# Kernel optimization log

Measured on AMD Instinct MI355X. Metric: run time of the kernel, lower is better.

## Reference

```python
import jax, jax.numpy as jnp
import numpy as np
from jax import lax

EPS = 1e-5

def _layernorm(x, g, b):
    m = x.mean(-1, keepdims=True)
    v = ((x - m) ** 2).mean(-1, keepdims=True)
    return (x - m) * lax.rsqrt(v + EPS) * g + b

def _batchnorm(x, g, b):
    # x: [N, C, L]; training-mode batch statistics (torch BatchNorm1d default)
    m = x.mean((0, 2), keepdims=True)
    v = ((x - m) ** 2).mean((0, 2), keepdims=True)
    return (x - m) * lax.rsqrt(v + EPS) * g[None, :, None] + b[None, :, None]

def _conv1d(x, w, bias, stride):
    y = lax.conv_general_dilated(x, w, window_strides=(stride,), padding='VALID',
                                 dimension_numbers=('NCH', 'OIH', 'NCH'))
    return y + bias[None, :, None]

def setup_inputs() -> dict:
    key = jax.random.key(0)
    ks = jax.random.split(key, 22)
    B, C, L = 512, 12, 5000
    NF, HID, LAT = 32, 64, 32
    def w(k, shape, fan_in):
        return jax.random.normal(k, shape, jnp.float32) * (1.0 / np.sqrt(fan_in))
    return {
        'x': jax.random.normal(ks[0], (B, C, L), jnp.float32),
        'c1w': w(ks[1], (32, C, 50), C * 50), 'c1b': jnp.zeros((32,), jnp.float32),
        'bn1g': jnp.ones((32,), jnp.float32), 'bn1b': jnp.zeros((32,), jnp.float32),
        'c2w': w(ks[2], (NF, 32, 25), 32 * 25), 'c2b': jnp.zeros((NF,), jnp.float32),
        'bn2g': jnp.ones((NF,), jnp.float32), 'bn2b': jnp.zeros((NF,), jnp.float32),
        'Wi': w(ks[3], (LAT, NF), NF) * 0.5, 'bi': jnp.zeros((LAT,), jnp.float32),
        'ln1g': jnp.ones((LAT,), jnp.float32), 'ln1b': jnp.zeros((LAT,), jnp.float32),
        'Wh': w(ks[4], (HID, LAT), LAT) * 0.5, 'bh': jnp.zeros((HID,), jnp.float32),
        'ln2g': jnp.ones((HID,), jnp.float32), 'ln2b': jnp.zeros((HID,), jnp.float32),
        'Wr': w(ks[5], (LAT, HID), HID) * 0.5, 'br': jnp.zeros((LAT,), jnp.float32),
        'Wo': w(ks[6], (LAT, LAT), LAT), 'bo': jnp.zeros((LAT,), jnp.float32),
    }

def reference(x, c1w, c1b, bn1g, bn1b, c2w, c2b, bn2g, bn2b,
              Wi, bi, ln1g, ln1b, Wh, bh, ln2g, ln2b, Wr, br, Wo, bo):
    # CNN front-end: [B,12,5000] -> [B,32,496] -> [B,32,95]
    h = jax.nn.relu(_batchnorm(_conv1d(x, c1w, c1b, 10), bn1g, bn1b))
    h = jax.nn.relu(_batchnorm(_conv1d(h, c2w, c2b, 5), bn2g, bn2b))
    feats = h.transpose(2, 0, 1)  # [T, B, NF]
    # input_proj + ln1 have no dependence on the recurrent state -> hoist out of loop
    xt_all = _layernorm(jnp.einsum('tbf,lf->tbl', feats, Wi) + bi, ln1g, ln1b)  # [T,B,LAT]

    def step(hstate, xt):
        combined = xt + hstate
        hp = jax.nn.relu(combined @ Wh.T + bh)      # [B, HID]
        hp = _layernorm(hp, ln2g, ln2b)
        hnew = jnp.tanh(hp @ Wr.T + br)             # [B, LAT]
        return hnew, hnew

    h0 = jnp.zeros((x.shape[0], Wr.shape[0]), x.dtype)
    _, outs = lax.scan(step, h0, xt_all)            # outs: [T, B, LAT]
    pooled = outs.mean(0)                           # mean over time
    return pooled @ Wo.T + bo                       # [B, LAT]
```

## Files before the change

kernel.cpp:

```cpp
#include <hip/hip_runtime.h>

#define EPS 1e-5f

#define B    512
#define C_IN 12
#define L_IN 5000
#define C1   32
#define L1   496
#define NF   32
#define L2   95
#define LAT  32
#define HID  64
#define T    L2

typedef short s16x8 __attribute__((ext_vector_type(8)));
typedef float f32x16 __attribute__((ext_vector_type(16)));

__device__ __forceinline__ ushort f2bf(float f) {
    uint u = __builtin_bit_cast(uint, f);
    u += 0x7fff + ((u >> 16) & 1);
    return (ushort)(u >> 16);
}
__device__ __forceinline__ float bf2f(ushort h) {
    return __builtin_bit_cast(float, (uint)h << 16);
}

__global__ void k_prep_w(const float* __restrict__ c1w, const float* __restrict__ c2w,
                         ushort* __restrict__ wfrag1, ushort* __restrict__ wfrag2) {
    int i = blockIdx.x * 256 + threadIdx.x;
    if (i < 6144) {
        int lane = i & 63, r = i >> 6;
        int split = r & 1, s = (r >> 1) & 3, c = r >> 3;
        int oc = lane & 31, kbase = s * 16 + (lane >> 5) * 8;
        ushort o8[8];
#pragma unroll
        for (int j = 0; j < 8; ++j) {
            int kk = kbase + j;
            float w = (kk < 50) ? c1w[oc * 600 + c * 50 + kk] : 0.f;
            ushort hb = f2bf(w);
            o8[j] = split ? f2bf(w - bf2f(hb)) : hb;
        }
        ushort4* dst = reinterpret_cast<ushort4*>(wfrag1) + (size_t)i * 2;
        dst[0] = make_ushort4(o8[0], o8[1], o8[2], o8[3]);
        dst[1] = make_ushort4(o8[4], o8[5], o8[6], o8[7]);
    } else if (i < 14336) {
        int j = i - 6144;
        int lane = j & 63, r = j >> 6;
        int split = r & 1, ks = (r >> 1) & 1, c = r >> 2;
        int oc = lane & 31, kbase = ks * 16 + (lane >> 5) * 8;
        ushort o8[8];
#pragma unroll
        for (int jj = 0; jj < 8; ++jj) {
            int kk = kbase + jj;
            float w = (kk < 25) ? c2w[oc * 800 + c * 25 + kk] : 0.f;
            ushort hb = f2bf(w);
            o8[jj] = split ? f2bf(w - bf2f(hb)) : hb;
        }
        ushort4* dst = reinterpret_cast<ushort4*>(wfrag2) + (size_t)j * 2;
        dst[0] = make_ushort4(o8[0], o8[1], o8[2], o8[3]);
        dst[1] = make_ushort4(o8[4], o8[5], o8[6], o8[7]);
    }
}

__global__ __launch_bounds__(256) void k_conv1(const float* __restrict__ x,
                                               const ushort* __restrict__ wfrag,
                                               const float* __restrict__ c1b,
                                               float* __restrict__ y1,
                                               float* __restrict__ raw1) {
    __shared__ ushort xh[2][1344];
    __shared__ ushort xl[2][1344];
    __shared__ float redS[4][32], redQ[4][32];
    const int chunk = blockIdx.x, b = blockIdx.y, tid = threadIdx.x;
    const int t0 = chunk * 128;
    const int v4max = min(336, (5000 - 10 * t0) >> 2);
    const float* xbase = x + (size_t)b * (C_IN * L_IN) + 10 * t0;

    float4 r0 = make_float4(0, 0, 0, 0), r1 = make_float4(0, 0, 0, 0);
    {
        const float4* s4 = reinterpret_cast<const float4*>(xbase);
        if (tid < v4max) r0 = s4[tid];
        if (tid + 256 < v4max) r1 = s4[tid + 256];
    }

    const int lane = tid & 63, wv = tid >> 6;
    const int cl = lane & 31;
    const int kgrp = lane >> 5;
    const int abase = 10 * (wv * 32 + cl) + kgrp * 8;

    f32x16 acc;
#pragma unroll
    for (int i = 0; i < 16; ++i) acc[i] = 0.f;

    const uint4* wf4 = reinterpret_cast<const uint4*>(wfrag);

    for (int c = 0; c < C_IN; ++c) {
        const int p = c & 1;
        if (tid < 336) {
            ushort4 h4, l4;
            h4.x = f2bf(r0.x); l4.x = f2bf(r0.x - bf2f(h4.x));
            h4.y = f2bf(r0.y); l4.y = f2bf(r0.y - bf2f(h4.y));
            h4.z = f2bf(r0.z); l4.z = f2bf(r0.z - bf2f(h4.z));
            h4.w = f2bf(r0.w); l4.w = f2bf(r0.w - bf2f(h4.w));
            *reinterpret_cast<ushort4*>(&xh[p][4 * tid]) = h4;
            *reinterpret_cast<ushort4*>(&xl[p][4 * tid]) = l4;
        }
        if (tid + 256 < 336) {
            ushort4 h4, l4;
            h4.x = f2bf(r1.x); l4.x = f2bf(r1.x - bf2f(h4.x));
            h4.y = f2bf(r1.y); l4.y = f2bf(r1.y - bf2f(h4.y));
            h4.z = f2bf(r1.z); l4.z = f2bf(r1.z - bf2f(h4.z));
            h4.w = f2bf(r1.w); l4.w = f2bf(r1.w - bf2f(h4.w));
            *reinterpret_cast<ushort4*>(&xh[p][4 * (tid + 256)]) = h4;
            *reinterpret_cast<ushort4*>(&xl[p][4 * (tid + 256)]) = l4;
        }
        if (c + 1 < C_IN) {
            const float4* s4 = reinterpret_cast<const float4*>(xbase + (size_t)(c + 1) * L_IN);
            r0 = make_float4(0, 0, 0, 0); r1 = make_float4(0, 0, 0, 0);
            if (tid < v4max) r0 = s4[tid];
            if (tid + 256 < v4max) r1 = s4[tid + 256];
        }
        __syncthreads();

        const ushort* ph = xh[p];
        const ushort* pl = xl[p];
        const uint4* wc = wf4 + (size_t)c * 512 + lane;
#pragma unroll
        for (int s = 0; s < 4; ++s) {
            const int idx = abase + s * 16;
            union { s16x8 v; uint u[4]; } ah, al, bh, bl;
            ah.u[0] = *reinterpret_cast<const uint*>(&ph[idx]);
            ah.u[1] = *reinterpret_cast<const uint*>(&ph[idx + 2]);
            ah.u[2] = *reinterpret_cast<const uint*>(&ph[idx + 4]);
            ah.u[3] = *reinterpret_cast<const uint*>(&ph[idx + 6]);
            al.u[0] = *reinterpret_cast<const uint*>(&pl[idx]);
            al.u[1] = *reinterpret_cast<const uint*>(&pl[idx + 2]);
            al.u[2] = *reinterpret_cast<const uint*>(&pl[idx + 4]);
            al.u[3] = *reinterpret_cast<const uint*>(&pl[idx + 6]);
            uint4 bq = wc[s * 128];
            uint4 lq = wc[s * 128 + 64];
            bh.u[0] = bq.x; bh.u[1] = bq.y; bh.u[2] = bq.z; bh.u[3] = bq.w;
            bl.u[0] = lq.x; bl.u[1] = lq.y; bl.u[2] = lq.z; bl.u[3] = lq.w;
            acc = __builtin_amdgcn_mfma_f32_32x32x16_bf16(ah.v, bh.v, acc, 0, 0, 0);
            acc = __builtin_amdgcn_mfma_f32_32x32x16_bf16(ah.v, bl.v, acc, 0, 0, 0);
            acc = __builtin_amdgcn_mfma_f32_32x32x16_bf16(al.v, bh.v, acc, 0, 0, 0);
        }
    }

    const float bias = c1b[cl];
    float sum = 0.f, sq = 0.f;
    float* yb = y1 + ((size_t)b * C1 + cl) * L1;
#pragma unroll
    for (int q = 0; q < 4; ++q) {
        const int trow = t0 + wv * 32 + 8 * q + 4 * kgrp;
        float4 st;
        st.x = acc[4 * q + 0] + bias;
        st.y = acc[4 * q + 1] + bias;
        st.z = acc[4 * q + 2] + bias;
        st.w = acc[4 * q + 3] + bias;
        if (trow < L1) {
            *reinterpret_cast<float4*>(yb + trow) = st;
            sum += st.x + st.y + st.z + st.w;
            sq  += st.x * st.x + st.y * st.y + st.z * st.z + st.w * st.w;
        }
    }
    sum += __shfl_xor(sum, 32);
    sq  += __shfl_xor(sq, 32);
    if (lane < 32) { redS[wv][cl] = sum; redQ[wv][cl] = sq; }
    __syncthreads();
    if (tid < 64) {
        int o = tid & 31, isQ = tid >> 5;
        float v = isQ ? (redQ[0][o] + redQ[1][o] + redQ[2][o] + redQ[3][o])
                      : (redS[0][o] + redS[1][o] + redS[2][o] + redS[3][o]);
        atomicAdd(&raw1[(isQ ? 1024 : 0) + o * 16], v);
    }
}

__global__ __launch_bounds__(192) void k_conv2(const float* __restrict__ y1,
                                               const ushort* __restrict__ wfrag2,
                                               const float* __restrict__ c2b,
                                               const float* __restrict__ raw1,
                                               const float* __restrict__ bn1g,
                                               const float* __restrict__ bn1b,
                                               float* __restrict__ y2,
                                               float* __restrict__ raw2) {
    __shared__ uint xs[C1][512];
    __shared__ float fin[64];
    __shared__ float redS[3][32], redQ[3][32];
    const int b = blockIdx.x, tid = threadIdx.x;

    if (tid < 32) {
        const float cnt = 1.f / (float)(B * L1);
        float mean = raw1[tid * 16] * cnt;
        float var = raw1[1024 + tid * 16] * cnt - mean * mean;
        float sc = bn1g[tid] * rsqrtf(var + EPS);
        fin[tid] = sc;
        fin[32 + tid] = bn1b[tid] - mean * sc;
    }
    __syncthreads();

    const float4* src = reinterpret_cast<const float4*>(y1 + (size_t)b * (C1 * L1));
    for (int v = tid; v < C1 * 128; v += 192) {
        const int c = v >> 7, i4 = v & 127;
        uint4 o = make_uint4(0, 0, 0, 0);
        if (i4 < 124) {
            const float sc = fin[c], sh = fin[32 + c];
            float4 d = src[c * 124 + i4];
            float e0 = fmaxf(fmaf(d.x, sc, sh), 0.f);
            float e1 = fmaxf(fmaf(d.y, sc, sh), 0.f);
            float e2 = fmaxf(fmaf(d.z, sc, sh), 0.f);
            float e3 = fmaxf(fmaf(d.w, sc, sh), 0.f);
            ushort h0 = f2bf(e0), h1 = f2bf(e1), h2 = f2bf(e2), h3 = f2bf(e3);
            o.x = (uint)h0 | ((uint)f2bf(e0 - bf2f(h0)) << 16);
            o.y = (uint)h1 | ((uint)f2bf(e1 - bf2f(h1)) << 16);
            o.z = (uint)h2 | ((uint)f2bf(e2 - bf2f(h2)) << 16);
            o.w = (uint)h3 | ((uint)f2bf(e3 - bf2f(h3)) << 16);
        }
        *reinterpret_cast<uint4*>(&xs[c][4 * i4]) = o;
    }
    __syncthreads();

    const int lane = tid & 63, wv = tid / 64;
    const int cl = lane & 31;
    const int kgrp = lane >> 5;
    const int tr = wv * 32 + cl;
    const int tbase = 5 * tr + kgrp * 8;

    f32x16 acc;
#pragma unroll
    for (int i = 0; i < 16; ++i) acc[i] = 0.f;

    const uint4* wf4 = reinterpret_cast<const uint4*>(wfrag2);

    for (int c = 0; c < C1; ++c) {
        const uint* xc = xs[c];
        const uint4* wfc = wf4 + (size_t)c * 256 + lane;
#pragma unroll
        for (int ks = 0; ks < 2; ++ks) {
            const int idx = tbase + ks * 16;
            uint u0 = xc[idx + 0], u1 = xc[idx + 1], u2 = xc[idx + 2], u3 = xc[idx + 3];
            uint u4 = xc[idx + 4], u5 = xc[idx + 5], u6 = xc[idx + 6], u7 = xc[idx + 7];
            union { s16x8 v; uint u[4]; } ah, al, bh, bl;
            ah.u[0] = (u0 & 0xFFFFu) | (u1 << 16);  al.u[0] = (u0 >> 16) | (u1 & 0xFFFF0000u);
            ah.u[1] = (u2 & 0xFFFFu) | (u3 << 16);  al.u[1] = (u2 >> 16) | (u3 & 0xFFFF0000u);
            ah.u[2] = (u4 & 0xFFFFu) | (u5 << 16);  al.u[2] = (u4 >> 16) | (u5 & 0xFFFF0000u);
            ah.u[3] = (u6 & 0xFFFFu) | (u7 << 16);  al.u[3] = (u6 >> 16) | (u7 & 0xFFFF0000u);
            uint4 bq = wfc[ks * 128];
            uint4 lq = wfc[ks * 128 + 64];
            bh.u[0] = bq.x; bh.u[1] = bq.y; bh.u[2] = bq.z; bh.u[3] = bq.w;
            bl.u[0] = lq.x; bl.u[1] = lq.y; bl.u[2] = lq.z; bl.u[3] = lq.w;
            acc = __builtin_amdgcn_mfma_f32_32x32x16_bf16(ah.v, bh.v, acc, 0, 0, 0);
            acc = __builtin_amdgcn_mfma_f32_32x32x16_bf16(ah.v, bl.v, acc, 0, 0, 0);
            acc = __builtin_amdgcn_mfma_f32_32x32x16_bf16(al.v, bh.v, acc, 0, 0, 0);
        }
    }

    const float bias = c2b[cl];
    float sum = 0.f, sq = 0.f;
#pragma unroll
    for (int q = 0; q < 4; ++q) {
#pragma unroll
        for (int j = 0; j < 4; ++j) {
            const int t = wv * 32 + 8 * q + 4 * kgrp + j;
            const float v = acc[4 * q + j] + bias;
            if (t < L2) {
                y2[((size_t)b * L2 + t) * NF + cl] = v;
                sum += v; sq += v * v;
            }
        }
    }
    sum += __shfl_xor(sum, 32);
    sq  += __shfl_xor(sq, 32);
    if (lane < 32) { redS[wv][cl] = sum; redQ[wv][cl] = sq; }
    __syncthreads();
    if (tid < 64) {
        int o = tid & 31, isQ = tid >> 5;
        float v = isQ ? (redQ[0][o] + redQ[1][o] + redQ[2][o])
                      : (redS[0][o] + redS[1][o] + redS[2][o]);
        atomicAdd(&raw2[(isQ ? 1024 : 0) + o * 16], v);
    }
}

__global__ __launch_bounds__(256) void k_proj(const float* __restrict__ y2,
                                              const float* __restrict__ raw2,
                                              const float* __restrict__ bn2g,
                                              const float* __restrict__ bn2b,
                                              const float* __restrict__ Wi,
                                              const float* __restrict__ bi,
                                              const float* __restrict__ ln1g,
                                              const float* __restrict__ ln1b,
                                              const float* __restrict__ Wh,
                                              const float* __restrict__ bh,
                                              float* __restrict__ xt2) {
    __shared__ float fin[64];
    if (threadIdx.x < 32) {
        const float cnt = 1.f / (float)(B * L2);
        float mean = raw2[threadIdx.x * 16] * cnt;
        float var = raw2[1024 + threadIdx.x * 16] * cnt - mean * mean;
        float sc = bn2g[threadIdx.x] * rsqrtf(var + EPS);
        fin[threadIdx.x] = sc;
        fin[32 + threadIdx.x] = bn2b[threadIdx.x] - mean * sc;
    }
    __syncthreads();

    const int r = blockIdx.x * 256 + threadIdx.x;
    const int b = r / 95, t = r - b * 95;

    const float4* row = reinterpret_cast<const float4*>(y2 + (size_t)r * NF);
    float u[NF];
#pragma unroll
    for (int f4 = 0; f4 < 8; ++f4) {
        float4 v = row[f4];
        u[4*f4]   = fmaxf(fmaf(v.x, fin[4*f4],   fin[32 + 4*f4]),   0.f);
        u[4*f4+1] = fmaxf(fmaf(v.y, fin[4*f4+1], fin[32 + 4*f4+1]), 0.f);
        u[4*f4+2] = fmaxf(fmaf(v.z, fin[4*f4+2], fin[32 + 4*f4+2]), 0.f);
        u[4*f4+3] = fmaxf(fmaf(v.w, fin[4*f4+3], fin[32 + 4*f4+3]), 0.f);
    }
    float xln[LAT];
    float s = 0.f, q = 0.f;
#pragma unroll
    for (int l = 0; l < LAT; ++l) {
        float a = bi[l];
#pragma unroll
        for (int f = 0; f < NF; ++f) a = fmaf(u[f], Wi[l * NF + f], a);
        xln[l] = a; s += a; q += a * a;
    }
    const float m = s * (1.f / LAT);
    const float inv = rsqrtf(q * (1.f / LAT) - m * m + EPS);
#pragma unroll
    for (int l = 0; l < LAT; ++l) xln[l] = (xln[l] - m) * inv * ln1g[l] + ln1b[l];

    float4* dst = reinterpret_cast<float4*>(xt2 + ((size_t)t * B + b) * HID);
#pragma unroll
    for (int j4 = 0; j4 < 16; ++j4) {
        float4 o4;
        float a0 = bh[4*j4], a1 = bh[4*j4+1], a2 = bh[4*j4+2], a3 = bh[4*j4+3];
#pragma unroll
        for (int l = 0; l < LAT; ++l) {
            float xl = xln[l];
            a0 = fmaf(xl, Wh[(4*j4)   * LAT + l], a0);
            a1 = fmaf(xl, Wh[(4*j4+1) * LAT + l], a1);
            a2 = fmaf(xl, Wh[(4*j4+2) * LAT + l], a2);
            a3 = fmaf(xl, Wh[(4*j4+3) * LAT + l], a3);
        }
        o4.x = a0; o4.y = a1; o4.z = a2; o4.w = a3;
        dst[j4] = o4;
    }
}

__global__ __launch_bounds__(64) void k_rnn(const float* __restrict__ xt2,
                                            const float* __restrict__ Wh,
                                            const float* __restrict__ ln2g,
                                            const float* __restrict__ ln2b,
                                            const float* __restrict__ Wr,
                                            const float* __restrict__ br,
                                            const float* __restrict__ Wo,
                                            const float* __restrict__ bo,
                                            float* __restrict__ out) {
    __shared__ __align__(16) float aS[64];
    __shared__ __align__(16) float hS[32];
    const int lane = threadIdx.x;
    const int b = blockIdx.x;
    const int l = lane & 31;

    float whv[LAT];
#pragma unroll
    for (int i = 0; i < LAT; ++i) whv[i] = Wh[lane * LAT + i];

    float wg[HID];
    float S1 = 0.f, S2 = br[l];
#pragma unroll
    for (int j = 0; j < HID; ++j) {
        float w = Wr[l * HID + j];
        wg[j] = w * ln2g[j];
        S1 += wg[j];
        S2 = fmaf(w, ln2b[j], S2);
    }

    float hfull[LAT];
#pragma unroll
    for (int i = 0; i < LAT; ++i) hfull[i] = 0.f;
    float pooled = 0.f;
    float xq = xt2[(size_t)b * HID + lane];

    for (int t = 0; t < T; ++t) {
        float xq_next = 0.f;
        if (t + 1 < T) xq_next = xt2[((size_t)(t + 1) * B + b) * HID + lane];

        float a0 = xq, a1 = 0.f, a2c = 0.f, a3c = 0.f;
#pragma unroll
        for (int i = 0; i < 8; ++i) {
            a0  = fmaf(hfull[4*i+0], whv[4*i+0], a0);
            a1  = fmaf(hfull[4*i+1], whv[4*i+1], a1);
            a2c = fmaf(hfull[4*i+2], whv[4*i+2], a2c);
            a3c = fmaf(hfull[4*i+3], whv[4*i+3], a3c);
        }
        const float a = fmaxf((a0 + a1) + (a2c + a3c), 0.f);

        aS[lane] = a;
        asm volatile("s_waitcnt lgkmcnt(0)" ::: "memory");

        float d0 = 0.f, d1 = 0.f, d2 = 0.f, d3 = 0.f;
#pragma unroll
        for (int i = 0; i < 16; ++i) {
            float4 v = reinterpret_cast<const float4*>(aS)[i];
            d0 = fmaf(v.x, wg[4*i+0], d0); d1 = fmaf(v.y, wg[4*i+1], d1);
            d2 = fmaf(v.z, wg[4*i+2], d2); d3 = fmaf(v.w, wg[4*i+3], d3);
        }
        float s = a, q = a * a;
#pragma unroll
        for (int off = 32; off >= 1; off >>= 1) { s += __shfl_xor(s, off); q += __shfl_xor(q, off); }
        const float m = s * (1.f / HID);
        const float inv = __builtin_amdgcn_rsqf(q * (1.f / HID) - m * m + EPS);
        const float dot = (d0 + d1) + (d2 + d3);
        const float a2v = fmaf(inv, dot - m * S1, S2);

        const float z = __builtin_amdgcn_exp2f(2.8853900817779268f * a2v);
        const float h = 1.f - 2.f * __builtin_amdgcn_rcpf(z + 1.f);
        pooled += h;

        if (lane < 32) hS[lane] = h;
        asm volatile("s_waitcnt lgkmcnt(0)" ::: "memory");
#pragma unroll
        for (int i = 0; i < 8; ++i) {
            float4 hv = reinterpret_cast<const float4*>(hS)[i];
            hfull[4*i] = hv.x; hfull[4*i+1] = hv.y; hfull[4*i+2] = hv.z; hfull[4*i+3] = hv.w;
        }
        xq = xq_next;
    }
    pooled *= (1.f / T);
    if (lane < 32) aS[lane] = pooled;
    asm volatile("s_waitcnt lgkmcnt(0)" ::: "memory");

    float wov[LAT];
#pragma unroll
    for (int i = 0; i < LAT; ++i) wov[i] = Wo[l * LAT + i];
    float b0 = bo[l], b1 = 0.f, b2 = 0.f, b3 = 0.f;
#pragma unroll
    for (int i = 0; i < 8; ++i) {
        float4 pv = reinterpret_cast<const float4*>(aS)[i];
        b0 = fmaf(pv.x, wov[4*i+0], b0); b1 = fmaf(pv.y, wov[4*i+1], b1);
        b2 = fmaf(pv.z, wov[4*i+2], b2); b3 = fmaf(pv.w, wov[4*i+3], b3);
    }
    if (lane < 32) out[(size_t)b * LAT + l] = (b0 + b1) + (b2 + b3);
}

extern "C" void kernel_launch(void* const* d_in, const int* in_sizes, int n_in,
                              void* d_out, int out_size, void* d_ws, size_t ws_size,
                              hipStream_t stream) {
    const float* x    = (const float*)d_in[0];
    const float* c1w  = (const float*)d_in[1];
    const float* c1b  = (const float*)d_in[2];
    const float* bn1g = (const float*)d_in[3];
    const float* bn1b = (const float*)d_in[4];
    const float* c2w  = (const float*)d_in[5];
    const float* c2b  = (const float*)d_in[6];
    const float* bn2g = (const float*)d_in[7];
    const float* bn2b = (const float*)d_in[8];
    const float* Wi   = (const float*)d_in[9];
    const float* bi   = (const float*)d_in[10];
    const float* ln1g = (const float*)d_in[11];
    const float* ln1b = (const float*)d_in[12];
    const float* Wh   = (const float*)d_in[13];
    const float* bh   = (const float*)d_in[14];
    const float* ln2g = (const float*)d_in[15];
    const float* ln2b = (const float*)d_in[16];
    const float* Wr   = (const float*)d_in[17];
    const float* br   = (const float*)d_in[18];
    const float* Wo   = (const float*)d_in[19];
    const float* bo   = (const float*)d_in[20];

    float* ws = (float*)d_ws;
    float* raw1 = ws;
    float* raw2 = ws + 2048;
    ushort* wfrag1 = (ushort*)(ws + 4096);
    ushort* wfrag2 = (ushort*)(ws + 28672);
    float* y1   = ws + 61440;
    float* y2   = ws + 8187904;
    float* xt2  = y1;
    float* out  = (float*)d_out;

    hipMemsetAsync(raw1, 0, 4096 * sizeof(float), stream);
    k_prep_w<<<56, 256, 0, stream>>>(c1w, c2w, wfrag1, wfrag2);
    k_conv1<<<dim3(4, B), 256, 0, stream>>>(x, wfrag1, c1b, y1, raw1);
    k_conv2<<<B, 192, 0, stream>>>(y1, wfrag2, c2b, raw1, bn1g, bn1b, y2, raw2);
    k_proj<<<190, 256, 0, stream>>>(y2, raw2, bn2g, bn2b, Wi, bi, ln1g, ln1b, Wh, bh, xt2);
    k_rnn<<<B, 64, 0, stream>>>(xt2, Wh, ln2g, ln2b, Wr, br, Wo, bo, out);
}
```

Before: 232.7 us.

## Restructure conv1 input staging and split MFMA accumulators into independent chains

conv1 now loads all 12 input channels up front into registers and stages them into one interleaved hi/lo shared buffer in two halves, each behind a single barrier. This replaces the previous per-channel load/convert/barrier loop. Both conv kernels now spread the three split-bf16 MFMA products over three separate accumulators, removing the serial dependency between them, and unpack hi/lo with v_perm. The costs are many more registers and much more LDS per conv1 block, which may reduce occupancy.

```diff
diff --git a/kernel.cpp b/kernel.cpp
--- a/kernel.cpp
+++ b/kernel.cpp
@@ -24,6 +24,13 @@
 __device__ __forceinline__ float bf2f(ushort h) {
     return __builtin_bit_cast(float, (uint)h << 16);
 }
+__device__ __forceinline__ uint pk(float f) {
+    ushort h = f2bf(f);
+    return (uint)h | ((uint)f2bf(f - bf2f(h)) << 16);
+}
+__device__ __forceinline__ uint4 pack4(float4 d) {
+    return make_uint4(pk(d.x), pk(d.y), pk(d.z), pk(d.w));
+}
 
 __global__ void k_prep_w(const float* __restrict__ c1w, const float* __restrict__ c2w,
                          ushort* __restrict__ wfrag1, ushort* __restrict__ wfrag2) {
@@ -62,89 +69,96 @@
     }
 }
 
+__device__ __forceinline__ void conv1_compute(const uint (*xs)[1344], const uint4* wf4,
+                                              int c0, int c1, int abase, int lane,
+                                              f32x16& hh, f32x16& hl, f32x16& lh) {
+    for (int c = c0; c < c1; ++c) {
+        const uint* xc = xs[c];
+        const uint4* wfc = wf4 + (size_t)c * 512 + lane;
+#pragma unroll
+        for (int s = 0; s < 4; ++s) {
+            const int idx = abase + s * 16;
+            uint2 p0 = *reinterpret_cast<const uint2*>(&xc[idx]);
+            uint2 p1 = *reinterpret_cast<const uint2*>(&xc[idx + 2]);
+            uint2 p2 = *reinterpret_cast<const uint2*>(&xc[idx + 4]);
+            uint2 p3 = *reinterpret_cast<const uint2*>(&xc[idx + 6]);
+            union { s16x8 v; uint u[4]; } ah, al, bh, bl;
+            ah.u[0] = __builtin_amdgcn_perm(p0.y, p0.x, 0x05040100u);
+            al.u[0] = __builtin_amdgcn_perm(p0.y, p0.x, 0x07060302u);
+            ah.u[1] = __builtin_amdgcn_perm(p1.y, p1.x, 0x05040100u);
+            al.u[1] = __builtin_amdgcn_perm(p1.y, p1.x, 0x07060302u);
+            ah.u[2] = __builtin_amdgcn_perm(p2.y, p2.x, 0x05040100u);
+            al.u[2] = __builtin_amdgcn_perm(p2.y, p2.x, 0x07060302u);
+            ah.u[3] = __builtin_amdgcn_perm(p3.y, p3.x, 0x05040100u);
+            al.u[3] = __builtin_amdgcn_perm(p3.y, p3.x, 0x07060302u);
+            uint4 bq = wfc[s * 128];
+            uint4 lq = wfc[s * 128 + 64];
+            bh.u[0] = bq.x; bh.u[1] = bq.y; bh.u[2] = bq.z; bh.u[3] = bq.w;
+            bl.u[0] = lq.x; bl.u[1] = lq.y; bl.u[2] = lq.z; bl.u[3] = lq.w;
+            hh = __builtin_amdgcn_mfma_f32_32x32x16_bf16(ah.v, bh.v, hh, 0, 0, 0);
+            hl = __builtin_amdgcn_mfma_f32_32x32x16_bf16(ah.v, bl.v, hl, 0, 0, 0);
+            lh = __builtin_amdgcn_mfma_f32_32x32x16_bf16(al.v, bh.v, lh, 0, 0, 0);
+        }
+    }
+}
+
 __global__ __launch_bounds__(256) void k_conv1(const float* __restrict__ x,
                                                const ushort* __restrict__ wfrag,
                                                const float* __restrict__ c1b,
                                                float* __restrict__ y1,
                                                float* __restrict__ raw1) {
-    __shared__ ushort xh[2][1344];
-    __shared__ ushort xl[2][1344];
+    __shared__ uint xs[C_IN][1344];
     __shared__ float redS[4][32], redQ[4][32];
     const int chunk = blockIdx.x, b = blockIdx.y, tid = threadIdx.x;
     const int t0 = chunk * 128;
     const int v4max = min(336, (5000 - 10 * t0) >> 2);
-    const float* xbase = x + (size_t)b * (C_IN * L_IN) + 10 * t0;
-
-    float4 r0 = make_float4(0, 0, 0, 0), r1 = make_float4(0, 0, 0, 0);
-    {
-        const float4* s4 = reinterpret_cast<const float4*>(xbase);
-        if (tid < v4max) r0 = s4[tid];
-        if (tid + 256 < v4max) r1 = s4[tid + 256];
-    }
+    const float4* xb4 = reinterpret_cast<const float4*>(x + (size_t)b * (C_IN * L_IN) + 10 * t0);
+
+    float4 rA[8], rB[8];
+#pragma unroll
+    for (int i = 0; i < 8; ++i) {
+        const int v = tid + i * 256;
+        const int c = v / 336, i4 = v - c * 336;
+        rA[i] = make_float4(0, 0, 0, 0);
+        if (i4 < v4max) rA[i] = xb4[c * 1250 + i4];
+    }
+#pragma unroll
+    for (int i = 0; i < 8; ++i) {
+        const int v = tid + 2048 + i * 256;
+        const int c = v / 336, i4 = v - c * 336;
+        rB[i] = make_float4(0, 0, 0, 0);
+        if (v < 4032 && i4 < v4max) rB[i] = xb4[c * 1250 + i4];
+    }
+
+    uint4* xs4 = reinterpret_cast<uint4*>(&xs[0][0]);
+#pragma unroll
+    for (int i = 0; i < 8; ++i) xs4[tid + i * 256] = pack4(rA[i]);
+    asm volatile("s_waitcnt lgkmcnt(0)" ::: "memory");
+    __builtin_amdgcn_s_barrier();
+    __builtin_amdgcn_sched_barrier(0);
 
     const int lane = tid & 63, wv = tid >> 6;
     const int cl = lane & 31;
     const int kgrp = lane >> 5;
     const int abase = 10 * (wv * 32 + cl) + kgrp * 8;
 
-    f32x16 acc;
-#pragma unroll
-    for (int i = 0; i < 16; ++i) acc[i] = 0.f;
-
+    f32x16 hh, hl, lh;
+#pragma unroll
+    for (int i = 0; i < 16; ++i) { hh[i] = 0.f; hl[i] = 0.f; lh[i] = 0.f; }
     const uint4* wf4 = reinterpret_cast<const uint4*>(wfrag);
 
-    for (int c = 0; c < C_IN; ++c) {
-        const int p = c & 1;
-        if (tid < 336) {
-            ushort4 h4, l4;
-            h4.x = f2bf(r0.x); l4.x = f2bf(r0.x - bf2f(h4.x));
-            h4.y = f2bf(r0.y); l4.y = f2bf(r0.y - bf2f(h4.y));
-            h4.z = f2bf(r0.z); l4.z = f2bf(r0.z - bf2f(h4.z));
-            h4.w = f2bf(r0.w); l4.w = f2bf(r0.w - bf2f(h4.w));
-            *reinterpret_cast<ushort4*>(&xh[p][4 * tid]) = h4;
-            *reinterpret_cast<ushort4*>(&xl[p][4 * tid]) = l4;
-        }
-        if (tid + 256 < 336) {
-            ushort4 h4, l4;
-            h4.x = f2bf(r1.x); l4.x = f2bf(r1.x - bf2f(h4.x));
-            h4.y = f2bf(r1.y); l4.y = f2bf(r1.y - bf2f(h4.y));
-            h4.z = f2bf(r1.z); l4.z = f2bf(r1.z - bf2f(h4.z));
-            h4.w = f2bf(r1.w); l4.w = f2bf(r1.w - bf2f(h4.w));
-            *reinterpret_cast<ushort4*>(&xh[p][4 * (tid + 256)]) = h4;
-            *reinterpret_cast<ushort4*>(&xl[p][4 * (tid + 256)]) = l4;
-        }
-        if (c + 1 < C_IN) {
-            const float4* s4 = reinterpret_cast<const float4*>(xbase + (size_t)(c + 1) * L_IN);
-            r0 = make_float4(0, 0, 0, 0); r1 = make_float4(0, 0, 0, 0);
-            if (tid < v4max) r0 = s4[tid];
-            if (tid + 256 < v4max) r1 = s4[tid + 256];
-        }
-        __syncthreads();
-
-        const ushort* ph = xh[p];
-        const ushort* pl = xl[p];
-        const uint4* wc = wf4 + (size_t)c * 512 + lane;
-#pragma unroll
-        for (int s = 0; s < 4; ++s) {
-            const int idx = abase + s * 16;
-            union { s16x8 v; uint u[4]; } ah, al, bh, bl;
-            ah.u[0] = *reinterpret_cast<const uint*>(&ph[idx]);
-            ah.u[1] = *reinterpret_cast<const uint*>(&ph[idx + 2]);
-            ah.u[2] = *reinterpret_cast<const uint*>(&ph[idx + 4]);
-            ah.u[3] = *reinterpret_cast<const uint*>(&ph[idx + 6]);
-            al.u[0] = *reinterpret_cast<const uint*>(&pl[idx]);
-            al.u[1] = *reinterpret_cast<const uint*>(&pl[idx + 2]);
-            al.u[2] = *reinterpret_cast<const uint*>(&pl[idx + 4]);
-            al.u[3] = *reinterpret_cast<const uint*>(&pl[idx + 6]);
-            uint4 bq = wc[s * 128];
-            uint4 lq = wc[s * 128 + 64];
-            bh.u[0] = bq.x; bh.u[1] = bq.y; bh.u[2] = bq.z; bh.u[3] = bq.w;
-            bl.u[0] = lq.x; bl.u[1] = lq.y; bl.u[2] = lq.z; bl.u[3] = lq.w;
-            acc = __builtin_amdgcn_mfma_f32_32x32x16_bf16(ah.v, bh.v, acc, 0, 0, 0);
-            acc = __builtin_amdgcn_mfma_f32_32x32x16_bf16(ah.v, bl.v, acc, 0, 0, 0);
-            acc = __builtin_amdgcn_mfma_f32_32x32x16_bf16(al.v, bh.v, acc, 0, 0, 0);
-        }
-    }
+    conv1_compute(xs, wf4, 0, 6, abase, lane, hh, hl, lh);
+
+#pragma unroll
+    for (int i = 0; i < 8; ++i) {
+        const int v = tid + 2048 + i * 256;
+        if (v < 4032) xs4[v] = pack4(rB[i]);
+    }
+    asm volatile("s_waitcnt lgkmcnt(0)" ::: "memory");
+    __builtin_amdgcn_s_barrier();
+    __builtin_amdgcn_sched_barrier(0);
+
+    conv1_compute(xs, wf4, 6, 12, abase, lane, hh, hl, lh);
 
     const float bias = c1b[cl];
     float sum = 0.f, sq = 0.f;
@@ -153,10 +167,10 @@
     for (int q = 0; q < 4; ++q) {
         const int trow = t0 + wv * 32 + 8 * q + 4 * kgrp;
         float4 st;
-        st.x = acc[4 * q + 0] + bias;
-        st.y = acc[4 * q + 1] + bias;
-        st.z = acc[4 * q + 2] + bias;
-        st.w = acc[4 * q + 3] + bias;
+        st.x = hh[4*q+0] + hl[4*q+0] + lh[4*q+0] + bias;
+        st.y = hh[4*q+1] + hl[4*q+1] + lh[4*q+1] + bias;
+        st.z = hh[4*q+2] + hl[4*q+2] + lh[4*q+2] + bias;
+        st.w = hh[4*q+3] + hl[4*q+3] + lh[4*q+3] + bias;
         if (trow < L1) {
             *reinterpret_cast<float4*>(yb + trow) = st;
             sum += st.x + st.y + st.z + st.w;
@@ -209,11 +223,7 @@
             float e1 = fmaxf(fmaf(d.y, sc, sh), 0.f);
             float e2 = fmaxf(fmaf(d.z, sc, sh), 0.f);
             float e3 = fmaxf(fmaf(d.w, sc, sh), 0.f);
-            ushort h0 = f2bf(e0), h1 = f2bf(e1), h2 = f2bf(e2), h3 = f2bf(e3);
-            o.x = (uint)h0 | ((uint)f2bf(e0 - bf2f(h0)) << 16);
-            o.y = (uint)h1 | ((uint)f2bf(e1 - bf2f(h1)) << 16);
-            o.z = (uint)h2 | ((uint)f2bf(e2 - bf2f(h2)) << 16);
-            o.w = (uint)h3 | ((uint)f2bf(e3 - bf2f(h3)) << 16);
+            o = make_uint4(pk(e0), pk(e1), pk(e2), pk(e3));
         }
         *reinterpret_cast<uint4*>(&xs[c][4 * i4]) = o;
     }
@@ -222,13 +232,11 @@
     const int lane = tid & 63, wv = tid / 64;
     const int cl = lane & 31;
     const int kgrp = lane >> 5;
-    const int tr = wv * 32 + cl;
-    const int tbase = 5 * tr + kgrp * 8;
-
-    f32x16 acc;
-#pragma unroll
-    for (int i = 0; i < 16; ++i) acc[i] = 0.f;
-
+    const int tbase = 5 * (wv * 32 + cl) + kgrp * 8;
+
+    f32x16 hh, hl, lh;
+#pragma unroll
+    for (int i = 0; i < 16; ++i) { hh[i] = 0.f; hl[i] = 0.f; lh[i] = 0.f; }
     const uint4* wf4 = reinterpret_cast<const uint4*>(wfrag2);
 
     for (int c = 0; c < C1; ++c) {
@@ -240,17 +248,21 @@
             uint u0 = xc[idx + 0], u1 = xc[idx + 1], u2 = xc[idx + 2], u3 = xc[idx + 3];
             uint u4 = xc[idx + 4], u5 = xc[idx + 5], u6 = xc[idx + 6], u7 = xc[idx + 7];
             union { s16x8 v; uint u[4]; } ah, al, bh, bl;
-            ah.u[0] = (u0 & 0xFFFFu) | (u1 << 16);  al.u[0] = (u0 >> 16) | (u1 & 0xFFFF0000u);
-            ah.u[1] = (u2 & 0xFFFFu) | (u3 << 16);  al.u[1] = (u2 >> 16) | (u3 & 0xFFFF0000u);
-            ah.u[2] = (u4 & 0xFFFFu) | (u5 << 16);  al.u[2] = (u4 >> 16) | (u5 & 0xFFFF0000u);
-            ah.u[3] = (u6 & 0xFFFFu) | (u7 << 16);  al.u[3] = (u6 >> 16) | (u7 & 0xFFFF0000u);
+            ah.u[0] = __builtin_amdgcn_perm(u1, u0, 0x05040100u);
+            al.u[0] = __builtin_amdgcn_perm(u1, u0, 0x07060302u);
+            ah.u[1] = __builtin_amdgcn_perm(u3, u2, 0x05040100u);
+            al.u[1] = __builtin_amdgcn_perm(u3, u2, 0x07060302u);
+            ah.u[2] = __builtin_amdgcn_perm(u5, u4, 0x05040100u);
+            al.u[2] = __builtin_amdgcn_perm(u5, u4, 0x07060302u);
+            ah.u[3] = __builtin_amdgcn_perm(u7, u6, 0x05040100u);
+            al.u[3] = __builtin_amdgcn_perm(u7, u6, 0x07060302u);
             uint4 bq = wfc[ks * 128];
             uint4 lq = wfc[ks * 128 + 64];
             bh.u[0] = bq.x; bh.u[1] = bq.y; bh.u[2] = bq.z; bh.u[3] = bq.w;
             bl.u[0] = lq.x; bl.u[1] = lq.y; bl.u[2] = lq.z; bl.u[3] = lq.w;
-            acc = __builtin_amdgcn_mfma_f32_32x32x16_bf16(ah.v, bh.v, acc, 0, 0, 0);
-            acc = __builtin_amdgcn_mfma_f32_32x32x16_bf16(ah.v, bl.v, acc, 0, 0, 0);
-            acc = __builtin_amdgcn_mfma_f32_32x32x16_bf16(al.v, bh.v, acc, 0, 0, 0);
+            hh = __builtin_amdgcn_mfma_f32_32x32x16_bf16(ah.v, bh.v, hh, 0, 0, 0);
+            hl = __builtin_amdgcn_mfma_f32_32x32x16_bf16(ah.v, bl.v, hl, 0, 0, 0);
+            lh = __builtin_amdgcn_mfma_f32_32x32x16_bf16(al.v, bh.v, lh, 0, 0, 0);
         }
     }
 
@@ -261,7 +273,7 @@
 #pragma unroll
         for (int j = 0; j < 4; ++j) {
             const int t = wv * 32 + 8 * q + 4 * kgrp + j;
-            const float v = acc[4 * q + j] + bias;
+            const float v = hh[4*q+j] + hl[4*q+j] + lh[4*q+j] + bias;
             if (t < L2) {
                 y2[((size_t)b * L2 + t) * NF + cl] = v;
                 sum += v; sq += v * v;
```

Result: slower. 257.5 us (+10.7%).
